# Optimization experiments

Measured on AMD Instinct MI355X. Metric: run time of the kernel, lower is better.

Reference implementation:

```python
import jax, jax.numpy as jnp
import numpy as np

INPUTS = 41024  # halfkp feature count (64 king squares * 641)
L1, L2, L3 = 128, 32, 32
B = 4096
ACTIVE_P = 30.0 / INPUTS  # ~30 active features per position


def setup_inputs() -> dict:
    key = jax.random.key(0)
    ks = jax.random.split(key, 10)
    # side-to-move indicators: us in {0,1}, them = 1 - us
    us = jax.random.randint(ks[0], (B, 1), 0, 2).astype(jnp.float32)
    them = 1.0 - us
    # sparse halfkp feature vectors (~30 active one-hot features per row)
    def sparse_feats(k):
        k1, k2 = jax.random.split(k)
        mask = jax.random.bernoulli(k1, ACTIVE_P, (B, INPUTS))
        return mask.astype(jnp.float32)
    w_in = sparse_feats(ks[1])
    b_in = sparse_feats(ks[2])
    s = 0.02
    W_ft = jax.random.normal(ks[3], (INPUTS, L1), dtype=jnp.float32) * s
    b_ft = jax.random.normal(ks[4], (L1,), dtype=jnp.float32) * s
    W1 = jax.random.normal(ks[5], (2 * L1, L2), dtype=jnp.float32) * s
    b1 = jax.random.normal(ks[6], (L2,), dtype=jnp.float32) * s
    W2 = jax.random.normal(ks[7], (L2, L3), dtype=jnp.float32) * s
    b2 = jax.random.normal(ks[8], (L3,), dtype=jnp.float32) * s
    Wo = jax.random.normal(ks[9], (L3, 1), dtype=jnp.float32) * s
    bo = jnp.zeros((1,), dtype=jnp.float32)
    return {"us": us, "them": them, "w_in": w_in, "b_in": b_in,
            "W_ft": W_ft, "b_ft": b_ft, "W1": W1, "b1": b1,
            "W2": W2, "b2": b2, "Wo": Wo, "bo": bo}


def reference(us, them, w_in, b_in, W_ft, b_ft, W1, b1, W2, b2, Wo, bo):
    # feature transformer (shared weights for white/black perspectives)
    w = w_in @ W_ft + b_ft  # [B, L1]
    b = b_in @ W_ft + b_ft  # [B, L1]
    l0 = us * jnp.concatenate([w, b], axis=1) + them * jnp.concatenate([b, w], axis=1)
    l0 = jnp.clip(l0, 0.0, 1.0)
    l1 = jnp.clip(l0 @ W1 + b1, 0.0, 1.0)
    l2 = jnp.clip(l1 @ W2 + b2, 0.0, 1.0)
    return l2 @ Wo + bo  # [B, 1]
```

## Files before the change

kernel.cpp:

```cpp
#include <hip/hip_runtime.h>

#define NNUE_INPUTS 41024
#define L1N 128
#define L2N 32
#define L3N 32
#define MAX_ACT 512
#define NC_ROW (NNUE_INPUTS / 4)
#define NC_HALF (NC_ROW / 2)
#define WITER 20

typedef float f4 __attribute__((ext_vector_type(4)));
typedef int   i4 __attribute__((ext_vector_type(4)));

__device__ __forceinline__ float clip01(float x) {
    return fminf(fmaxf(x, 0.0f), 1.0f);
}

__device__ __forceinline__ int nzbits(const f4& x) {
    const i4 b = *(const i4*)&x;
    return (b[0] | b[1]) | (b[2] | b[3]);
}

__global__ __launch_bounds__(256, 6) void nnue_fused_kernel(
    const float* __restrict__ us, const float* __restrict__ them,
    const float* __restrict__ w_in, const float* __restrict__ b_in,
    const float* __restrict__ W_ft, const float* __restrict__ b_ft,
    const float* __restrict__ W1, const float* __restrict__ b1,
    const float* __restrict__ W2, const float* __restrict__ b2,
    const float* __restrict__ Wo, const float* __restrict__ bo,
    float* __restrict__ out)
{
    __shared__ int   s_idx_w[MAX_ACT];
    __shared__ int   s_idx_b[MAX_ACT];
    __shared__ int   s_cnt[2];
    __shared__ float s_w[L1N];
    __shared__ float s_b[L1N];
    __shared__ float s_l0[2 * L1N];
    __shared__ float s_part[8][L2N];
    __shared__ float s_l1[L2N];
    __shared__ float s_l2[L3N];

    const int row  = blockIdx.x;
    const int tid  = threadIdx.x;
    const int wave = tid >> 6;
    const int lane = tid & 63;

    if (tid < 2) s_cnt[tid] = 0;
    const float u = us[row];
    const float t = them[row];
    __syncthreads();

    {
        const int     p    = wave >> 1;
        const f4*     src  = (const f4*)((p ? b_in : w_in) + (size_t)row * NNUE_INPUTS);
        int*          mcnt = &s_cnt[p];
        int*          midx = p ? s_idx_b : s_idx_w;
        const int     base = (wave & 1) * NC_HALF;

        auto emitf4 = [&](const f4& x, int c) {
            const i4 b = *(const i4*)&x;
            const int e = c * 4;
            if (b[0]) { int q = atomicAdd(mcnt, 1); midx[q & (MAX_ACT - 1)] = e;     }
            if (b[1]) { int q = atomicAdd(mcnt, 1); midx[q & (MAX_ACT - 1)] = e + 1; }
            if (b[2]) { int q = atomicAdd(mcnt, 1); midx[q & (MAX_ACT - 1)] = e + 2; }
            if (b[3]) { int q = atomicAdd(mcnt, 1); midx[q & (MAX_ACT - 1)] = e + 3; }
        };

        int c = base + lane;
        f4 x0 = __builtin_nontemporal_load(src + c);
        f4 x1 = __builtin_nontemporal_load(src + c + 64);
        f4 x2 = __builtin_nontemporal_load(src + c + 128);
        f4 x3 = __builtin_nontemporal_load(src + c + 192);
        #pragma unroll 1
        for (int i = 0; i < WITER - 1; ++i) {
            const int cn = c + 256;
            const f4 n0 = __builtin_nontemporal_load(src + cn);
            const f4 n1 = __builtin_nontemporal_load(src + cn + 64);
            const f4 n2 = __builtin_nontemporal_load(src + cn + 128);
            const f4 n3 = __builtin_nontemporal_load(src + cn + 192);
            if (nzbits(x0)) emitf4(x0, c);
            if (nzbits(x1)) emitf4(x1, c + 64);
            if (nzbits(x2)) emitf4(x2, c + 128);
            if (nzbits(x3)) emitf4(x3, c + 192);
            x0 = n0; x1 = n1; x2 = n2; x3 = n3;
            c = cn;
        }
        if (nzbits(x0)) emitf4(x0, c);
        if (nzbits(x1)) emitf4(x1, c + 64);
        if (nzbits(x2)) emitf4(x2, c + 128);
        if (nzbits(x3)) emitf4(x3, c + 192);
        if (lane < NC_HALF - WITER * 256) {
            const int ct = base + WITER * 256 + lane;
            const f4 x = __builtin_nontemporal_load(src + ct);
            if (nzbits(x)) emitf4(x, ct);
        }
    }
    __syncthreads();

    const int kw = min(s_cnt[0], MAX_ACT);
    const int kb = min(s_cnt[1], MAX_ACT);

    {
        const int  ch   = tid & (L1N - 1);
        const bool is_b = tid >= L1N;
        const int* lst  = is_b ? s_idx_b : s_idx_w;
        const int  K    = is_b ? kb : kw;
        const float* Wc = W_ft + ch;
        float acc = b_ft[ch];
        int k = 0;
        for (; k + 8 <= K; k += 8) {
            const float f0 = Wc[(size_t)lst[k]     * L1N];
            const float f1 = Wc[(size_t)lst[k + 1] * L1N];
            const float f2 = Wc[(size_t)lst[k + 2] * L1N];
            const float f3 = Wc[(size_t)lst[k + 3] * L1N];
            const float f4v = Wc[(size_t)lst[k + 4] * L1N];
            const float f5 = Wc[(size_t)lst[k + 5] * L1N];
            const float f6 = Wc[(size_t)lst[k + 6] * L1N];
            const float f7 = Wc[(size_t)lst[k + 7] * L1N];
            acc += ((f0 + f1) + (f2 + f3)) + ((f4v + f5) + (f6 + f7));
        }
        for (; k + 4 <= K; k += 4) {
            const float f0 = Wc[(size_t)lst[k]     * L1N];
            const float f1 = Wc[(size_t)lst[k + 1] * L1N];
            const float f2 = Wc[(size_t)lst[k + 2] * L1N];
            const float f3 = Wc[(size_t)lst[k + 3] * L1N];
            acc += (f0 + f1) + (f2 + f3);
        }
        for (; k < K; ++k) acc += Wc[(size_t)lst[k] * L1N];
        if (is_b) s_b[ch] = acc; else s_w[ch] = acc;
    }
    __syncthreads();

    if (tid < L1N) {
        const float wv = s_w[tid], bv = s_b[tid];
        s_l0[tid]       = clip01(u * wv + t * bv);
        s_l0[L1N + tid] = clip01(u * bv + t * wv);
    }
    __syncthreads();

    {
        const int o  = tid & 31;
        const int ch = tid >> 5;
        float a = 0.0f;
        const int k0 = ch * 32;
        #pragma unroll
        for (int k = 0; k < 32; ++k) a += s_l0[k0 + k] * W1[(k0 + k) * L2N + o];
        s_part[ch][o] = a;
    }
    __syncthreads();
    if (tid < L2N) {
        float a = b1[tid];
        #pragma unroll
        for (int j = 0; j < 8; ++j) a += s_part[j][tid];
        s_l1[tid] = clip01(a);
    }
    __syncthreads();

    if (tid < L3N) {
        float a = b2[tid];
        #pragma unroll
        for (int k = 0; k < L2N; ++k) a += s_l1[k] * W2[k * L3N + tid];
        s_l2[tid] = clip01(a);
    }
    __syncthreads();

    if (tid == 0) {
        float a = bo[0];
        #pragma unroll
        for (int k = 0; k < L3N; ++k) a += s_l2[k] * Wo[k];
        out[row] = a;
    }
}

extern "C" void kernel_launch(void* const* d_in, const int* in_sizes, int n_in,
                              void* d_out, int out_size, void* d_ws, size_t ws_size,
                              hipStream_t stream) {
    const float* us   = (const float*)d_in[0];
    const float* them = (const float*)d_in[1];
    const float* w_in = (const float*)d_in[2];
    const float* b_in = (const float*)d_in[3];
    const float* W_ft = (const float*)d_in[4];
    const float* b_ft = (const float*)d_in[5];
    const float* W1   = (const float*)d_in[6];
    const float* b1   = (const float*)d_in[7];
    const float* W2   = (const float*)d_in[8];
    const float* b2   = (const float*)d_in[9];
    const float* Wo   = (const float*)d_in[10];
    const float* bo   = (const float*)d_in[11];
    float* out = (float*)d_out;

    const int B = in_sizes[0];
    nnue_fused_kernel<<<dim3(B), dim3(256), 0, stream>>>(
        us, them, w_in, b_in, W_ft, b_ft, W1, b1, W2, b2, Wo, bo, out);
}
```

Baseline: 1.206 ms.

## Split fused NNUE kernel into grid-wide sparse scan and per-row eval kernels

Replaces the single per-row fused kernel with three launches: a counter-zeroing kernel, a grid-stride scan over both dense input matrices that writes the active feature indices of each row to workspace using global atomics, and an eval kernel that gathers W_ft rows and runs the small MLP. The aim is to stream the large sparse inputs at full bandwidth, independent of the per-row block structure. The cost is extra launches, global atomics and a workspace round trip. Indices beyond 128 per row wrap, and the eval kernel copies all 128 index slots even when fewer were written. The original fused path is kept as a fallback when workspace is too small, and its 8-wide gather unroll is removed.

```diff
diff --git a/kernel.cpp b/kernel.cpp
--- a/kernel.cpp
+++ b/kernel.cpp
@@ -4,8 +4,9 @@
 #define L1N 128
 #define L2N 32
 #define L3N 32
+#define NC_ROW (NNUE_INPUTS / 4)
+#define MAXK 128
 #define MAX_ACT 512
-#define NC_ROW (NNUE_INPUTS / 4)
 #define NC_HALF (NC_ROW / 2)
 #define WITER 20
 
@@ -19,6 +20,147 @@
 __device__ __forceinline__ int nzbits(const f4& x) {
     const i4 b = *(const i4*)&x;
     return (b[0] | b[1]) | (b[2] | b[3]);
+}
+
+__global__ void zero_cnt_kernel(int* __restrict__ cnt, int n) {
+    const int i = blockIdx.x * blockDim.x + threadIdx.x;
+    if (i < n) cnt[i] = 0;
+}
+
+__global__ __launch_bounds__(256, 8) void scan_kernel(
+    const float* __restrict__ w_in, const float* __restrict__ b_in,
+    int* __restrict__ cnt, int* __restrict__ idx, int nrows)
+{
+    const int p = blockIdx.y;
+    const f4* __restrict__ src = (const f4*)(p ? b_in : w_in);
+    int* __restrict__ cntp = cnt + p * nrows;
+    int* __restrict__ idxp = idx + (size_t)p * nrows * MAXK;
+
+    const int nch    = nrows * NC_ROW;
+    const int stride = gridDim.x * blockDim.x;
+
+    auto emit = [&](const f4& x, int c) {
+        const i4 b = *(const i4*)&x;
+        if ((b[0] | b[1]) | (b[2] | b[3])) {
+            const int row = c / NC_ROW;
+            const int e0  = (c - row * NC_ROW) << 2;
+            int* __restrict__ cp = cntp + row;
+            int* __restrict__ ip = idxp + row * MAXK;
+            if (b[0]) { int q = atomicAdd(cp, 1); ip[q & (MAXK - 1)] = e0;     }
+            if (b[1]) { int q = atomicAdd(cp, 1); ip[q & (MAXK - 1)] = e0 + 1; }
+            if (b[2]) { int q = atomicAdd(cp, 1); ip[q & (MAXK - 1)] = e0 + 2; }
+            if (b[3]) { int q = atomicAdd(cp, 1); ip[q & (MAXK - 1)] = e0 + 3; }
+        }
+    };
+
+    int c = blockIdx.x * blockDim.x + threadIdx.x;
+    for (; c + 3 * stride < nch; c += 4 * stride) {
+        const f4 x0 = __builtin_nontemporal_load(src + c);
+        const f4 x1 = __builtin_nontemporal_load(src + c + stride);
+        const f4 x2 = __builtin_nontemporal_load(src + c + 2 * stride);
+        const f4 x3 = __builtin_nontemporal_load(src + c + 3 * stride);
+        emit(x0, c);
+        emit(x1, c + stride);
+        emit(x2, c + 2 * stride);
+        emit(x3, c + 3 * stride);
+    }
+    for (; c < nch; c += stride) {
+        const f4 x = __builtin_nontemporal_load(src + c);
+        emit(x, c);
+    }
+}
+
+__global__ __launch_bounds__(256, 8) void eval_kernel(
+    const float* __restrict__ us, const float* __restrict__ them,
+    const float* __restrict__ W_ft, const float* __restrict__ b_ft,
+    const float* __restrict__ W1, const float* __restrict__ b1,
+    const float* __restrict__ W2, const float* __restrict__ b2,
+    const float* __restrict__ Wo, const float* __restrict__ bo,
+    const int* __restrict__ cnt, const int* __restrict__ idx,
+    float* __restrict__ out, int nrows)
+{
+    __shared__ int   s_idx[2][MAXK];
+    __shared__ float s_w[L1N];
+    __shared__ float s_b[L1N];
+    __shared__ float s_l0[2 * L1N];
+    __shared__ float s_part[8][L2N];
+    __shared__ float s_l1[L2N];
+    __shared__ float s_l2[L3N];
+
+    const int row = blockIdx.x;
+    const int tid = threadIdx.x;
+
+    const int kw = min(cnt[row], MAXK);
+    const int kb = min(cnt[nrows + row], MAXK);
+    const float u = us[row];
+    const float t = them[row];
+
+    {
+        const int p = tid >> 7;
+        const int j = tid & (MAXK - 1);
+        s_idx[p][j] = idx[((size_t)p * nrows + row) * MAXK + j];
+    }
+    __syncthreads();
+
+    {
+        const int  ch   = tid & (L1N - 1);
+        const bool is_b = tid >= L1N;
+        const int* lst  = s_idx[is_b ? 1 : 0];
+        const int  K    = is_b ? kb : kw;
+        const float* Wc = W_ft + ch;
+        float acc = b_ft[ch];
+        int k = 0;
+        for (; k + 4 <= K; k += 4) {
+            const float f0 = Wc[(size_t)lst[k]     * L1N];
+            const float f1 = Wc[(size_t)lst[k + 1] * L1N];
+            const float f2 = Wc[(size_t)lst[k + 2] * L1N];
+            const float f3 = Wc[(size_t)lst[k + 3] * L1N];
+            acc += (f0 + f1) + (f2 + f3);
+        }
+        for (; k < K; ++k) acc += Wc[(size_t)lst[k] * L1N];
+        if (is_b) s_b[ch] = acc; else s_w[ch] = acc;
+    }
+    __syncthreads();
+
+    if (tid < L1N) {
+        const float wv = s_w[tid], bv = s_b[tid];
+        s_l0[tid]       = clip01(u * wv + t * bv);
+        s_l0[L1N + tid] = clip01(u * bv + t * wv);
+    }
+    __syncthreads();
+
+    {
+        const int o  = tid & 31;
+        const int ch = tid >> 5;
+        float a = 0.0f;
+        const int k0 = ch * 32;
+        #pragma unroll
+        for (int k = 0; k < 32; ++k) a += s_l0[k0 + k] * W1[(k0 + k) * L2N + o];
+        s_part[ch][o] = a;
+    }
+    __syncthreads();
+    if (tid < L2N) {
+        float a = b1[tid];
+        #pragma unroll
+        for (int j = 0; j < 8; ++j) a += s_part[j][tid];
+        s_l1[tid] = clip01(a);
+    }
+    __syncthreads();
+
+    if (tid < L3N) {
+        float a = b2[tid];
+        #pragma unroll
+        for (int k = 0; k < L2N; ++k) a += s_l1[k] * W2[k * L3N + tid];
+        s_l2[tid] = clip01(a);
+    }
+    __syncthreads();
+
+    if (tid == 0) {
+        float a = bo[0];
+        #pragma unroll
+        for (int k = 0; k < L3N; ++k) a += s_l2[k] * Wo[k];
+        out[row] = a;
+    }
 }
 
 __global__ __launch_bounds__(256, 6) void nnue_fused_kernel(
@@ -108,17 +250,6 @@
         const float* Wc = W_ft + ch;
         float acc = b_ft[ch];
         int k = 0;
-        for (; k + 8 <= K; k += 8) {
-            const float f0 = Wc[(size_t)lst[k]     * L1N];
-            const float f1 = Wc[(size_t)lst[k + 1] * L1N];
-            const float f2 = Wc[(size_t)lst[k + 2] * L1N];
-            const float f3 = Wc[(size_t)lst[k + 3] * L1N];
-            const float f4v = Wc[(size_t)lst[k + 4] * L1N];
-            const float f5 = Wc[(size_t)lst[k + 5] * L1N];
-            const float f6 = Wc[(size_t)lst[k + 6] * L1N];
-            const float f7 = Wc[(size_t)lst[k + 7] * L1N];
-            acc += ((f0 + f1) + (f2 + f3)) + ((f4v + f5) + (f6 + f7));
-        }
         for (; k + 4 <= K; k += 4) {
             const float f0 = Wc[(size_t)lst[k]     * L1N];
             const float f1 = Wc[(size_t)lst[k + 1] * L1N];
@@ -190,6 +321,17 @@
     float* out = (float*)d_out;
 
     const int B = in_sizes[0];
-    nnue_fused_kernel<<<dim3(B), dim3(256), 0, stream>>>(
-        us, them, w_in, b_in, W_ft, b_ft, W1, b1, W2, b2, Wo, bo, out);
-}
+
+    const size_t need = ((size_t)2 * B + (size_t)2 * B * MAXK) * sizeof(int);
+    if (d_ws != nullptr && ws_size >= need) {
+        int* cnt = (int*)d_ws;
+        int* idx = cnt + 2 * B;
+        zero_cnt_kernel<<<dim3((2 * B + 255) / 256), dim3(256), 0, stream>>>(cnt, 2 * B);
+        scan_kernel<<<dim3(2048, 2), dim3(256), 0, stream>>>(w_in, b_in, cnt, idx, B);
+        eval_kernel<<<dim3(B), dim3(256), 0, stream>>>(
+            us, them, W_ft, b_ft, W1, b1, W2, b2, Wo, bo, cnt, idx, out, B);
+    } else {
+        nnue_fused_kernel<<<dim3(B), dim3(256), 0, stream>>>(
+            us, them, w_in, b_in, W_ft, b_ft, W1, b1, W2, b2, Wo, bo, out);
+    }
+}
```

After: 1.252 ms. +3.8%, slower.
